# Kernel optimization log

Measured on AMD Instinct MI355X. Metric: run time of the kernel, lower is better.

## Reference

```python
import jax, jax.numpy as jnp
import numpy as np

P = 16        # patch size
IMG = 224     # image H=W
C = 3         # channels
D = 768       # projection_dim (= patch flatten dim here)
H = 12        # num heads
M = D // 4    # new_size = flattened_size / shrink_ratio(4) = 192
L = 6         # transformer layers
N = (IMG // P) ** 2   # 196 patches
FF = 3072     # dense_units[0]
HEAD = 512    # dense_units[2]
NCLS = 1000
EPS = 1e-6
B = 32


def setup_inputs() -> dict:
    key = jax.random.key(0)
    ks = iter(jax.random.split(key, 40))
    u = lambda shape, s=0.02: jax.random.uniform(next(ks), shape, jnp.float32, -s, s)
    image = jax.random.normal(next(ks), (B, IMG, IMG, C), jnp.float32)
    return dict(
        image=image,
        patch_w=u((P * P * C, D)), patch_b=u((D,)), pos_emb=u((N, D)),
        qw=u((L, D, M, H)), qb=jnp.zeros((L, M, H), jnp.float32),
        kw=u((L, D, M, H)), kb=jnp.zeros((L, M, H), jnp.float32),
        vw=u((L, D, M, H)), vb=jnp.zeros((L, M, H), jnp.float32),
        ow1=u((L, H * N, N)), ob1=jnp.zeros((L, M, N), jnp.float32),
        ow2=u((L, M, D)), ob2=jnp.zeros((L, N, D), jnp.float32),
        d1w=u((L, D, FF)), d1b=u((L, FF)),
        d2w=u((L, FF, D)), d2b=u((L, D)),
        head_w=u((N * D, HEAD), 0.005), head_b=u((HEAD,)),
        cls_w=u((HEAD, NCLS)), cls_b=u((NCLS,)),
    )


def _ln(x):
    # ViT_Custom_LayerNormalization: moments over axes [0,1,2] (all elements of [B,N,D])
    m = jnp.mean(x)
    v = jnp.mean(jnp.square(x - m))
    return (x - m) / jnp.sqrt(v + EPS)


def _gelu(x):
    return jax.nn.gelu(x, approximate=False)  # keras 'gelu' default is exact


def _forward(image, patch_w, patch_b, pos_emb, qw, qb, kw, kb, vw, vb,
             ow1, ob1, ow2, ob2, d1w, d1b, d2w, d2b, head_w, head_b, cls_w, cls_b):
    b = image.shape[0]
    # tf.image.extract_patches with VALID, stride=patch: [B,N,p*p*C] row-major patches
    patches = image.reshape(b, IMG // P, P, IMG // P, P, C)
    patches = patches.transpose(0, 1, 3, 2, 4, 5).reshape(b, N, P * P * C)
    x = patches @ patch_w + patch_b + pos_emb  # patch encode + pos embedding
    scale = 1.0 / np.float32(np.sqrt(D))       # key_dim = projection_dim
    for l in range(L):
        x1 = _ln(x)
        # per-head 3-D tensordot projections: [B,N,D] x [D,M,H] -> [B,N,M,H]
        q = jnp.einsum('bnd,dmh->bnmh', x1, qw[l]) + qb[l]
        k = jnp.einsum('bnd,dmh->bnmh', x1, kw[l]) + kb[l]
        v = jnp.einsum('bnd,dmh->bnmh', x1, vw[l]) + vb[l]
        att = jnp.einsum('bnmh,bNmh->bhnN', q, k) * scale  # [B,H,N,N]
        a = jax.nn.softmax(att, axis=-1)
        # attn @ V, then the module's transpose/unstack-concat -> [B,M,H*N] head-major
        o = jnp.einsum('bhnN,bNmh->bmhn', a, v).reshape(b, M, H * N)
        t = (o @ ow1[l] + ob1[l]).transpose(0, 2, 1)  # [B,N,M]
        attn_out = t @ ow2[l] + ob2[l]                # [B,N,D]
        x2 = attn_out + x
        x3 = _ln(x2)
        h = _gelu(x3 @ d1w[l] + d1b[l])
        h = _gelu(h @ d2w[l] + d2b[l])
        x = h + x2
    x = _ln(x)
    flat = x.reshape(b, N * D)
    feat = _gelu(flat @ head_w + head_b)
    return feat @ cls_w + cls_b  # [B, NCLS]


def reference(image, patch_w, patch_b, pos_emb, qw, qb, kw, kb, vw, vb,
              ow1, ob1, ow2, ob2, d1w, d1b, d2w, d2b, head_w, head_b, cls_w, cls_b):
    return _forward(image, patch_w, patch_b, pos_emb, qw, qb, kw, kb, vw, vb,
                    ow1, ob1, ow2, ob2, d1w, d1b, d2w, d2b, head_w, head_b, cls_w, cls_b)
```

## Files before the change

kernel.cpp:

```cpp
#include <hip/hip_runtime.h>
#include <cmath>

#define BZ    32
#define NP    196
#define DDIM  768
#define NHEAD 12
#define MDIM  192
#define NLAY  6
#define FFDIM 3072
#define HEADU 512
#define NCLS  1000
#define KHEAD 150528
#define BND   4816896

typedef __bf16 bf16_t;
typedef __bf16 bf16x8 __attribute__((ext_vector_type(8)));
typedef __bf16 bf16x4 __attribute__((ext_vector_type(4)));
typedef float  f32x4  __attribute__((ext_vector_type(4)));
typedef float  f32x2  __attribute__((ext_vector_type(2)));

#define OB_X      0L
#define OB_R      19267584L
#define OB_XB     38535168L
#define OB_XQKV   48168960L
#define OB_VT     134873088L
#define OB_O      165543936L
#define OB_T      194641920L
#define OB_WQKV   197050368L
#define OB_WO1    260751360L
#define OB_WO2    268025856L
#define OB_WD1    269795328L
#define OB_WD2    298106880L
#define OB_WPAT   326418432L
#define OB_BQKV   327598080L
#define OB_OB1T   327763968L
#define OB_RED    328667136L
#define OB_FEAT   328675584L

#define VT_SSTRIDE  39936L
#define ATTN_LDSP   93184
#define ATTN_LDS    143360
#define XROW        13824

__device__ __forceinline__ float gelu_exact(float x){
    return 0.5f * x * (1.0f + erff(x * 0.70710678118654752f));
}

__device__ __forceinline__ void gld16(const void* g, void* l){
    __builtin_amdgcn_global_load_lds((const __attribute__((address_space(1))) void*)g,
                                     (__attribute__((address_space(3))) void*)l, 16, 0, 0);
}

__global__ void __launch_bounds__(256)
patch_extract_k(const float* __restrict__ img, bf16_t* __restrict__ out)
{
    long idx = (long)blockIdx.x * 256 + threadIdx.x;
    if (idx >= (long)BND) return;
    int k = (int)(idx % DDIM);
    long bn = idx / DDIM;
    int n = (int)(bn % NP);
    int b = (int)(bn / NP);
    int c  = k % 3;
    int pj = (k / 3) % 16;
    int pi = k / 48;
    int gi = n / 14, gj = n % 14;
    long src = (((long)(b * 224 + gi * 16 + pi)) * 224 + (gj * 16 + pj)) * 3 + c;
    out[idx] = (bf16_t)img[src];
}

__global__ void __launch_bounds__(256)
wconv_k(const float* __restrict__ in, bf16_t* __restrict__ out,
        int IR, int IC, long OLD, int perm, int padTo, long inZ, long outZ)
{
    __shared__ float tile[32][33];
    int tid = threadIdx.x, tx = tid & 31, ty = tid >> 5;
    int c0 = blockIdx.x * 32, r0 = blockIdx.y * 32;
    const float* inz = in + (long)blockIdx.z * inZ;
    bf16_t* outz = out + (long)blockIdx.z * outZ;
    #pragma unroll
    for (int i = 0; i < 4; i++){
        int r = r0 + ty + 8*i, c = c0 + tx;
        tile[ty + 8*i][tx] = (r < IR && c < IC) ? inz[(long)r * IC + c] : 0.f;
    }
    __syncthreads();
    #pragma unroll
    for (int i = 0; i < 4; i++){
        int c = c0 + ty + 8*i, r = r0 + tx;
        if (c < IC && r < padTo){
            long pc = perm ? (long)(c % 12) * 192 + c / 12 : (long)c;
            outz[pc * OLD + r] = (bf16_t)tile[tx][ty + 8*i];
        }
    }
}

__global__ void __launch_bounds__(256)
gather_bias_k(const float* __restrict__ qb, const float* __restrict__ kb,
              const float* __restrict__ vb, float* __restrict__ out)
{
    int tid = blockIdx.x * 256 + threadIdx.x;
    int l = blockIdx.y;
    if (tid >= 6912) return;
    int g = tid / 2304, w = tid % 2304;
    int h = w / 192, m = w % 192;
    const float* src = (g == 0) ? qb : (g == 1) ? kb : vb;
    out[l*6912 + tid] = src[l*2304 + m * 12 + h];
}

__global__ void __launch_bounds__(256)
tr_bias_k(const float* __restrict__ ob1, float* __restrict__ out)
{
    int idx = blockIdx.x * 256 + threadIdx.x;
    int l = blockIdx.y;
    if (idx >= 37632) return;
    int n = idx / 192, m = idx - n*192;
    out[(long)l*37632 + idx] = ob1[(long)l*37632 + m*196 + n];
}

__global__ void __launch_bounds__(256)
zero_pad_o_k(bf16_t* __restrict__ o)
{
    int idx = blockIdx.x * 256 + threadIdx.x;
    if (idx >= 6144*16) return;
    int r = idx >> 4, j = idx & 15;
    o[(long)r * 2368 + 2352 + j] = (bf16_t)0.f;
}

__global__ void __launch_bounds__(256)
tr_v_k(const bf16_t* __restrict__ X, bf16_t* __restrict__ VT)
{
    __shared__ bf16_t tile[32][33];
    int tid = threadIdx.x, tx = tid & 31, ty = tid >> 5;
    int s = blockIdx.z, b = s & 31, h = s >> 5;
    int m0 = blockIdx.x * 32, n0 = blockIdx.y * 32;
    #pragma unroll
    for (int i = 0; i < 4; i++){
        int r = n0 + ty + 8*i, c = m0 + tx;
        tile[ty + 8*i][tx] = (r < 196) ?
            X[(long)(b*196 + r) * 6912 + 4608 + h*192 + c] : (bf16_t)0.f;
    }
    __syncthreads();
    #pragma unroll
    for (int i = 0; i < 4; i++){
        int m = m0 + ty + 8*i, n = n0 + tx;
        if (n < 208)
            VT[(long)s * VT_SSTRIDE + (long)m * 208 + n] = tile[tx][ty + 8*i];
    }
}

__global__ void __launch_bounds__(256)
reduce_k(const float* __restrict__ x, float* __restrict__ psum, float* __restrict__ psq)
{
    __shared__ float ss[256], sq[256];
    float s = 0.f, q = 0.f;
    const long n4 = BND / 4;
    const float4* x4 = (const float4*)x;
    for (long i = (long)blockIdx.x * 256 + threadIdx.x; i < n4; i += (long)gridDim.x * 256){
        float4 v = x4[i];
        s += v.x + v.y + v.z + v.w;
        q += v.x*v.x + v.y*v.y + v.z*v.z + v.w*v.w;
    }
    ss[threadIdx.x] = s; sq[threadIdx.x] = q;
    __syncthreads();
    for (int st = 128; st > 0; st >>= 1){
        if (threadIdx.x < st){ ss[threadIdx.x] += ss[threadIdx.x+st]; sq[threadIdx.x] += sq[threadIdx.x+st]; }
        __syncthreads();
    }
    if (threadIdx.x == 0){ psum[blockIdx.x] = ss[0]; psq[blockIdx.x] = sq[0]; }
}

__global__ void __launch_bounds__(256)
ln_apply_k(const float* __restrict__ x, bf16_t* __restrict__ yb, float* __restrict__ yf,
           const float* __restrict__ psum, const float* __restrict__ psq)
{
    __shared__ float sred[8];
    int tid = threadIdx.x;
    float s = 0.f, q = 0.f;
    for (int i = tid; i < 1024; i += 256){ s += psum[i]; q += psq[i]; }
    #pragma unroll
    for (int off = 32; off > 0; off >>= 1){ s += __shfl_xor(s, off); q += __shfl_xor(q, off); }
    if ((tid & 63) == 0){ sred[(tid>>6)*2] = s; sred[(tid>>6)*2+1] = q; }
    __syncthreads();
    s = sred[0] + sred[2] + sred[4] + sred[6];
    q = sred[1] + sred[3] + sred[5] + sred[7];
    float mean = s / (float)BND;
    float inv  = rsqrtf(q / (float)BND - mean*mean + 1e-6f);

    long i = (long)blockIdx.x * 256 + tid;
    if (i >= BND / 4) return;
    float4 v = ((const float4*)x)[i];
    v.x = (v.x - mean) * inv;
    v.y = (v.y - mean) * inv;
    v.z = (v.z - mean) * inv;
    v.w = (v.w - mean) * inv;
    bf16x4 o4 = { (bf16_t)v.x, (bf16_t)v.y, (bf16_t)v.z, (bf16_t)v.w };
    ((bf16x4*)yb)[i] = o4;
    if (yf) ((float4*)yf)[i] = v;
}

__global__ void __launch_bounds__(256)
attn_fused_k(const bf16_t* __restrict__ XQKV, const bf16_t* __restrict__ VT,
             bf16_t* __restrict__ O)
{
    extern __shared__ char lds[];
    const int tid = threadIdx.x, lane = tid & 63, w = tid >> 6;
    const int fr = lane & 15, kc = lane >> 4;
    const int s = blockIdx.y, qhalf = blockIdx.x;
    const int q0 = qhalf * 112;
    const int b = s & 31, h = s >> 5;
    const float scale = 0.03608439182435161f;
    const char* Xb = (const char*)XQKV + (long)(b*196) * XROW;
    const char* Qs = Xb + h*384;
    const char* Ks = Xb + 4608 + h*384;
    const char* Vs = (const char*)(VT + (long)s * VT_SSTRIDE);

    for (int t = 0; t < 23; t++){
        int idx = t*256 + tid;
        if (idx < 5824){
            int row = idx / 28, sl = idx - row*28;
            bool val = (sl < 24) && (row < 196);
            const char* src = Ks + (val ? ((long)row*XROW + ((sl*16) ^ ((row & 7) << 4))) : 0);
            gld16(src, lds + idx*16);
        }
    }
    asm volatile("s_waitcnt vmcnt(0)");
    __syncthreads();

    float pv_all[2][13][4];
    #pragma unroll
    for (int ii = 0; ii < 2; ii++){
        int i = w + ii*4;
        if (i >= 7) continue;
        f32x4 sa[13];
        #pragma unroll
        for (int f = 0; f < 13; f++) sa[f] = (f32x4){0.f,0.f,0.f,0.f};
        int qr = q0 + i*16 + fr; if (qr > 195) qr = 195;
        #pragma unroll
        for (int c = 0; c < 6; c++){
            bf16x8 av = *(const bf16x8*)(Qs + (long)qr*XROW + c*64 + kc*16);
            #pragma unroll
            for (int f = 0; f < 13; f++){
                int krow = f*16 + fr;
                bf16x8 bv = *(const bf16x8*)(lds + krow*448 + ((c*64 + kc*16) ^ ((krow & 7) << 4)));
                sa[f] = __builtin_amdgcn_mfma_f32_16x16x32_bf16(av, bv, sa[f], 0, 0, 0);
            }
        }
        #pragma unroll
        for (int r = 0; r < 4; r++){
            float mx = -1e30f;
            #pragma unroll
            for (int f = 0; f < 13; f++)
                if (f*16 + fr < 196) mx = fmaxf(mx, sa[f][r] * scale);
            mx = fmaxf(mx, __shfl_xor(mx, 1));
            mx = fmaxf(mx, __shfl_xor(mx, 2));
            mx = fmaxf(mx, __shfl_xor(mx, 4));
            mx = fmaxf(mx, __shfl_xor(mx, 8));
            float sum = 0.f;
            #pragma unroll
            for (int f = 0; f < 13; f++){
                float pv = (f*16 + fr < 196) ? __expf(sa[f][r] * scale - mx) : 0.f;
                pv_all[ii][f][r] = pv; sum += pv;
            }
            sum += __shfl_xor(sum, 1);
            sum += __shfl_xor(sum, 2);
            sum += __shfl_xor(sum, 4);
            sum += __shfl_xor(sum, 8);
            float inv = 1.f / sum;
            #pragma unroll
            for (int f = 0; f < 13; f++) pv_all[ii][f][r] *= inv;
        }
        #pragma unroll
        for (int f = 0; f < 13; f++)
            #pragma unroll
            for (int r = 0; r < 4; r++){
                int row = i*16 + kc*4 + r;
                int cb = (f*16 + fr) * 2;
                int a = ATTN_LDSP + row*448 + (cb < 384 ? (cb ^ ((row & 7) << 4)) : cb);
                *(bf16_t*)(lds + a) = (bf16_t)pv_all[ii][f][r];
            }
        if (lane < 32){
            int row = i*16 + (lane >> 1);
            *(f32x4*)(lds + ATTN_LDSP + row*448 + 416 + (lane & 1)*16) = (f32x4){0.f,0.f,0.f,0.f};
        }
    }
    __syncthreads();

    for (int t = 0; t < 21; t++){
        int idx = t*256 + tid;
        int row = idx / 28, sl = idx - row*28;
        bool val = (sl < 26);
        int cb = (sl < 24) ? ((sl*16) ^ ((row & 7) << 4)) : sl*16;
        const char* src = Vs + (val ? (row*416 + cb) : 0);
        gld16(src, lds + idx*16);
    }
    asm volatile("s_waitcnt vmcnt(0)");
    __syncthreads();

    f32x4 oa2[2][12];
    #pragma unroll
    for (int ii = 0; ii < 2; ii++){
        int i = w + ii*4;
        #pragma unroll
        for (int f = 0; f < 12; f++) oa2[ii][f] = (f32x4){0.f,0.f,0.f,0.f};
        if (i >= 7) continue;
        #pragma unroll
        for (int c = 0; c < 7; c++){
            int prow = i*16 + fr;
            int cb = c*64 + kc*16;
            int acb = (cb < 384) ? (cb ^ ((prow & 7) << 4)) : cb;
            bf16x8 av = *(const bf16x8*)(lds + ATTN_LDSP + prow*448 + acb);
            #pragma unroll
            for (int f = 0; f < 12; f++){
                int vrow = f*16 + fr;
                int bcb = (cb < 384) ? (cb ^ ((vrow & 7) << 4)) : cb;
                bf16x8 bv = *(const bf16x8*)(lds + vrow*448 + bcb);
                oa2[ii][f] = __builtin_amdgcn_mfma_f32_16x16x32_bf16(av, bv, oa2[ii][f], 0, 0, 0);
            }
        }
    }
    __syncthreads();

    #pragma unroll
    for (int ii = 0; ii < 2; ii++){
        int i = w + ii*4;
        if (i >= 7) continue;
        #pragma unroll
        for (int f = 0; f < 12; f++){
            int m = f*16 + fr;
            #pragma unroll
            for (int r = 0; r < 4; r++){
                int nl = i*16 + kc*4 + r;
                *(bf16_t*)(lds + m*232 + nl*2) = (bf16_t)oa2[ii][f][r];
            }
        }
    }
    __syncthreads();
    const int nch = (qhalf == 0) ? 28 : 21;
    const int total = 192 * nch;
    char* ob = (char*)O + ((long)(b*192))*4736 + ((long)(h*196 + q0))*2;
    for (int idx = tid; idx < total; idx += 256){
        int m = idx / nch, ch = idx - m*nch;
        f32x2 v2 = *(const f32x2*)(lds + m*232 + ch*8);
        *(f32x2*)(ob + (long)m*4736 + ch*8) = v2;
    }
}

__global__ void __launch_bounds__(256)
mfma_gemm_k(const bf16_t* __restrict__ A, long ldA, long sA,
            const bf16_t* __restrict__ B, long ldB, long sB,
            void* __restrict__ C, long ldC, long sC,
            const float* __restrict__ Cadd,
            const float* __restrict__ bias1,
            const float* __restrict__ bias2, int b2mod, int b2ld,
            int Md, int Nd, int Kd, float alpha, int doGelu, int mode)
{
    __shared__ bf16_t sm[3][2][128][32];
    const int tid = threadIdx.x;
    const int lane = tid & 63, w = tid >> 6;
    const int wm = w >> 1, wn = w & 1;
    const int z = blockIdx.z;

    int n2d = gridDim.x * gridDim.y;
    int flat = blockIdx.x + gridDim.x * blockIdx.y;
    int q8 = n2d >> 3, r8 = n2d & 7;
    int xcd = flat & 7, pos = flat >> 3;
    int id2 = (xcd < r8 ? xcd*(q8+1) : r8*(q8+1) + (xcd-r8)*q8) + pos;
    int bx = id2 % gridDim.x, by = id2 / gridDim.x;

    const int row0 = by * 128, col0 = bx * 128;

    const bf16_t* Ab = A + (long)z * sA + (long)row0 * ldA;
    const bf16_t* Bb = B + (long)z * sB + (long)col0 * ldB;

    f32x4 acc[4][4];
    #pragma unroll
    for (int i = 0; i < 4; i++)
        #pragma unroll
        for (int j = 0; j < 4; j++)
            acc[i][j] = (f32x4){0.f, 0.f, 0.f, 0.f};

    const int fr = lane & 15, kc = lane >> 4;
    const int swz = (fr >> 1) & 3;
    int aOff[4], bOff[4];
    #pragma unroll
    for (int i = 0; i < 4; i++){
        aOff[i] = (wm*64 + i*16 + fr) * 64 + ((kc ^ swz) << 4);
        bOff[i] = (wn*64 + i*16 + fr) * 64 + ((kc ^ swz) << 4);
    }

    auto stage = [&](int buf, int kt){
        long kOff = (long)kt * 32;
        #pragma unroll
        for (int r = 0; r < 2; r++){
            int idx = r*256 + tid;
            int row = idx >> 2, cp = idx & 3;
            int cc = cp ^ ((row >> 1) & 3);
            gld16((const void*)(Ab + (long)row*ldA + kOff + cc*8), (void*)&sm[buf][0][row][cp*8]);
            gld16((const void*)(Bb + (long)row*ldB + kOff + cc*8), (void*)&sm[buf][1][row][cp*8]);
        }
    };

    const int nt = Kd >> 5;
    stage(0, 0);
    stage(1, 1);
    asm volatile("s_waitcnt vmcnt(4)" ::: "memory");
    __builtin_amdgcn_s_barrier();
    __builtin_amdgcn_sched_barrier(0);

    for (int t = 0; t < nt; t++){
        int cur = t % 3;
        if (t + 2 < nt) stage((t + 2) % 3, t + 2);
        const char* baseA = (const char*)sm + cur * 16384;
        const char* baseB = baseA + 8192;
        bf16x8 av[4], bv[4];
        #pragma unroll
        for (int i = 0; i < 4; i++){
            av[i] = *(const bf16x8*)(baseA + aOff[i]);
            bv[i] = *(const bf16x8*)(baseB + bOff[i]);
        }
        __builtin_amdgcn_s_setprio(1);
        #pragma unroll
        for (int i = 0; i < 4; i++)
            #pragma unroll
            for (int j = 0; j < 4; j++)
                acc[i][j] = __builtin_amdgcn_mfma_f32_16x16x32_bf16(av[i], bv[j], acc[i][j], 0, 0, 0);
        __builtin_amdgcn_s_setprio(0);
        if (t + 2 < nt)      asm volatile("s_waitcnt vmcnt(4)" ::: "memory");
        else if (t + 1 < nt) asm volatile("s_waitcnt vmcnt(0)" ::: "memory");
        __builtin_amdgcn_s_barrier();
        __builtin_amdgcn_sched_barrier(0);
    }

    #pragma unroll
    for (int i = 0; i < 4; i++){
        int gmb = row0 + wm*64 + i*16 + kc*4;
        #pragma unroll
        for (int j = 0; j < 4; j++){
            int gn = col0 + wn*64 + j*16 + fr;
            if (gn >= Nd) continue;
            #pragma unroll
            for (int r = 0; r < 4; r++){
                int gm = gmb + r;
                if (gm >= Md) continue;
                float v = alpha * acc[i][j][r];
                if (bias1) v += bias1[gn];
                if (bias2) v += bias2[(long)(gm % b2mod) * b2ld + gn];
                if (doGelu) v = gelu_exact(v);
                if (mode == 0){
                    long off = (long)z*sC + (long)gm*ldC + gn;
                    if (Cadd) v += Cadd[off];
                    ((float*)C)[off] = v;
                } else {
                    ((bf16_t*)C)[(long)z*sC + (long)gm*ldC + gn] = (bf16_t)v;
                }
            }
        }
    }
}

__global__ void __launch_bounds__(256)
head_splitk_k(const float* __restrict__ A, const float* __restrict__ W, float* __restrict__ feat)
{
    __shared__ float As[16][36];
    __shared__ float Bs[16][68];
    int col0 = blockIdx.x * 64;
    long kbase = (long)blockIdx.y * 2352;
    int tid = threadIdx.x, tx = tid & 15, ty = tid >> 4;
    float acc[2][4] = {};
    for (int k0 = 0; k0 < 2352; k0 += 16){
        #pragma unroll
        for (int u = 0; u < 2; u++){
            int idx = tid * 2 + u;
            int m = idx >> 4, kk = idx & 15;
            As[kk][m] = A[(long)m * KHEAD + kbase + k0 + kk];
        }
        #pragma unroll
        for (int u = 0; u < 4; u++){
            int idx = tid * 4 + u;
            int kk = idx >> 6, n = idx & 63;
            Bs[kk][n] = W[(kbase + k0 + kk) * 512 + col0 + n];
        }
        __syncthreads();
        #pragma unroll
        for (int kk = 0; kk < 16; kk++){
            float a0 = As[kk][ty*2], a1 = As[kk][ty*2+1];
            float b0 = Bs[kk][tx*4], b1 = Bs[kk][tx*4+1], b2 = Bs[kk][tx*4+2], b3 = Bs[kk][tx*4+3];
            acc[0][0] += a0*b0; acc[0][1] += a0*b1; acc[0][2] += a0*b2; acc[0][3] += a0*b3;
            acc[1][0] += a1*b0; acc[1][1] += a1*b1; acc[1][2] += a1*b2; acc[1][3] += a1*b3;
        }
        __syncthreads();
    }
    #pragma unroll
    for (int i = 0; i < 2; i++)
        #pragma unroll
        for (int j = 0; j < 4; j++)
            atomicAdd(&feat[(ty*2 + i) * 512 + col0 + tx*4 + j], acc[i][j]);
}

__global__ void __launch_bounds__(256)
head_finish_k(float* __restrict__ feat, const float* __restrict__ hb)
{
    int i = blockIdx.x * 256 + threadIdx.x;
    if (i < BZ * HEADU) feat[i] = gelu_exact(feat[i] + hb[i & 511]);
}

__global__ void __launch_bounds__(256)
cls_k(const float* __restrict__ feat, const float* __restrict__ W,
      const float* __restrict__ bias, float* __restrict__ out)
{
    __shared__ float fs[512];
    int b = blockIdx.y;
    int j = blockIdx.x * 256 + threadIdx.x;
    for (int i = threadIdx.x; i < 512; i += 256) fs[i] = feat[b * 512 + i];
    __syncthreads();
    if (j < NCLS){
        float s = bias[j];
        for (int k = 0; k < 512; k++) s += fs[k] * W[(long)k * NCLS + j];
        out[b * NCLS + j] = s;
    }
}

extern "C" void kernel_launch(void* const* d_in, const int* in_sizes, int n_in,
                              void* d_out, int out_size, void* d_ws, size_t ws_size,
                              hipStream_t stream)
{
    const float* image   = (const float*)d_in[0];
    const float* patch_w = (const float*)d_in[1];
    const float* patch_b = (const float*)d_in[2];
    const float* pos_emb = (const float*)d_in[3];
    const float* qw  = (const float*)d_in[4];
    const float* qb  = (const float*)d_in[5];
    const float* kw  = (const float*)d_in[6];
    const float* kb  = (const float*)d_in[7];
    const float* vw  = (const float*)d_in[8];
    const float* vb  = (const float*)d_in[9];
    const float* ow1 = (const float*)d_in[10];
    const float* ob1 = (const float*)d_in[11];
    const float* ow2 = (const float*)d_in[12];
    const float* ob2 = (const float*)d_in[13];
    const float* d1w = (const float*)d_in[14];
    const float* d1b = (const float*)d_in[15];
    const float* d2w = (const float*)d_in[16];
    const float* d2b = (const float*)d_in[17];
    const float* head_w = (const float*)d_in[18];
    const float* head_b = (const float*)d_in[19];
    const float* cls_w  = (const float*)d_in[20];
    const float* cls_b  = (const float*)d_in[21];

    char* wsb = (char*)d_ws;
    float*  X    = (float*) (wsb + OB_X);
    float*  R    = (float*) (wsb + OB_R);
    bf16_t* XB   = (bf16_t*)(wsb + OB_XB);
    bf16_t* XQKV = (bf16_t*)(wsb + OB_XQKV);
    bf16_t* VT   = (bf16_t*)(wsb + OB_VT);
    bf16_t* O    = (bf16_t*)(wsb + OB_O);
    bf16_t* Tt   = (bf16_t*)(wsb + OB_T);
    bf16_t* H1   = XQKV;
    bf16_t* PATB = XQKV;
    bf16_t* WQKV = (bf16_t*)(wsb + OB_WQKV);
    bf16_t* WO1  = (bf16_t*)(wsb + OB_WO1);
    bf16_t* WO2  = (bf16_t*)(wsb + OB_WO2);
    bf16_t* WD1  = (bf16_t*)(wsb + OB_WD1);
    bf16_t* WD2  = (bf16_t*)(wsb + OB_WD2);
    bf16_t* WPAT = (bf16_t*)(wsb + OB_WPAT);
    float*  BQKV = (float*) (wsb + OB_BQKV);
    float*  OB1T = (float*) (wsb + OB_OB1T);
    float*  RSUM = (float*) (wsb + OB_RED);
    float*  RSQ  = RSUM + 1024;
    float*  FEAT = (float*) (wsb + OB_FEAT);
    float*  out  = (float*)d_out;

    hipFuncSetAttribute((const void*)attn_fused_k,
                        hipFuncAttributeMaxDynamicSharedMemorySize, ATTN_LDS);

    auto mg = [&](const bf16_t* A, long ldA, long sA, const bf16_t* B, long ldB, long sB,
                  void* C, long ldC, long sC, const float* Cadd, const float* b1,
                  const float* b2, int b2mod, int b2ld,
                  int Md, int Nd, int Kd, int nb, float alpha, int gelu, int mode){
        dim3 g((Nd + 127) / 128, (Md + 127) / 128, nb);
        mfma_gemm_k<<<g, 256, 0, stream>>>(A, ldA, sA, B, ldB, sB, C, ldC, sC,
                                           Cadd, b1, b2, b2mod, b2ld,
                                           Md, Nd, Kd, alpha, gelu, mode);
    };
    auto wconv = [&](const float* in, bf16_t* o_, int IR, int IC, int perm, long OLD,
                     int padTo, int nz, long inZ, long outZ){
        dim3 g((IC + 31) / 32, (padTo + 31) / 32, nz);
        wconv_k<<<g, 256, 0, stream>>>(in, o_, IR, IC, OLD, perm, padTo, inZ, outZ);
    };
    auto layernorm = [&](const float* in, bf16_t* ob, float* of){
        reduce_k<<<1024, 256, 0, stream>>>(in, RSUM, RSQ);
        ln_apply_k<<<4704, 256, 0, stream>>>(in, ob, of, RSUM, RSQ);
    };

    wconv(patch_w, WPAT, 768, 768, 0, 768, 768, 1, 0, 0);
    wconv(qw, WQKV,               768, 2304, 1, 768, 768, 6, 768L*2304, 6912L*768);
    wconv(kw, WQKV + 2304L*768,   768, 2304, 1, 768, 768, 6, 768L*2304, 6912L*768);
    wconv(vw, WQKV + 4608L*768,   768, 2304, 1, 768, 768, 6, 768L*2304, 6912L*768);
    wconv(ow1, WO1, 2352, 196, 0, 2368, 2368, 6, 2352L*196, 606208L);
    wconv(ow2, WO2, 192, 768, 0, 192, 192, 6, 147456L, 147456L);
    wconv(d1w, WD1, 768, 3072, 0, 768, 768, 6, 2359296L, 2359296L);
    wconv(d2w, WD2, 3072, 768, 0, 3072, 3072, 6, 2359296L, 2359296L);
    gather_bias_k<<<dim3(27, 6), 256, 0, stream>>>(qb, kb, vb, BQKV);
    tr_bias_k<<<dim3(147, 6), 256, 0, stream>>>(ob1, OB1T);

    patch_extract_k<<<18816, 256, 0, stream>>>(image, PATB);
    mg(PATB, 768, 0, WPAT, 768, 0, X, 768, 0,
       nullptr, patch_b, pos_emb, 196, 768, 6272, 768, 768, 1, 1.f, 0, 0);
    zero_pad_o_k<<<384, 256, 0, stream>>>(O);

    for (int l = 0; l < NLAY; l++){
        layernorm(X, XB, nullptr);
        mg(XB, 768, 0, WQKV + (long)l*6912*768, 768, 0, XQKV, 6912, 0, nullptr,
           BQKV + l*6912, nullptr, 1, 1, 6272, 6912, 768, 1, 1.f, 0, 1);
        tr_v_k<<<dim3(6, 7, 384), 256, 0, stream>>>(XQKV, VT);
        attn_fused_k<<<dim3(2, 384), 256, ATTN_LDS, stream>>>(XQKV, VT, O);
        mg(WO1 + (long)l*606208, 2368, 0, O, 2368, 192L*2368, Tt, 192, 37632,
           nullptr, nullptr, OB1T + (long)l*37632, 196, 192,
           196, 192, 2368, 32, 1.f, 0, 1);
        mg(Tt, 192, 0, WO2 + (long)l*147456, 192, 0, R, 768, 0, X, nullptr,
           ob2 + (long)l*196*768, 196, 768, 6272, 768, 192, 1, 1.f, 0, 0);
        layernorm(R, XB, nullptr);
        mg(XB, 768, 0, WD1 + (long)l*2359296, 768, 0, H1, 3072, 0, nullptr,
           d1b + l*3072, nullptr, 1, 1, 6272, 3072, 768, 1, 1.f, 1, 1);
        mg(H1, 3072, 0, WD2 + (long)l*2359296, 3072, 0, X, 768, 0, R,
           d2b + l*768, nullptr, 1, 1, 6272, 768, 3072, 1, 1.f, 1, 0);
    }

    layernorm(X, XB, R);
    hipMemsetAsync(FEAT, 0, BZ * HEADU * sizeof(float), stream);
    head_splitk_k<<<dim3(8, 64), 256, 0, stream>>>(R, head_w, FEAT);
    head_finish_k<<<64, 256, 0, stream>>>(FEAT, head_b);
    cls_k<<<dim3(4, 32), 256, 0, stream>>>(FEAT, cls_w, cls_b, out);
    (void)in_sizes; (void)n_in; (void)out_size; (void)ws_size;
}
```

Measured before the change: 3.426 ms.

## Fuse layernorm statistics into GEMM epilogues and add small-tile GEMM for ow1

Each fp32-output GEMM that produces the residual stream now accumulates per-block sum and sum-of-squares in its epilogue and writes partials, so the separate full-tensor reduction kernel before each layernorm is removed. The batched ow1 projection uses a new 64x64-tile MFMA kernel, which raises block count for the small 196x192 per-batch problem. The head GELU+bias is folded into the classifier kernel. The cost is extra epilogue work and a block-level sync in the main GEMM. The sum-of-squares variance is kept, and partials are now summed over 294 blocks.

```diff
diff --git a/kernel.cpp b/kernel.cpp
--- a/kernel.cpp
+++ b/kernel.cpp
@@ -12,6 +12,7 @@
 #define NCLS  1000
 #define KHEAD 150528
 #define BND   4816896
+#define NPART 294
 
 typedef __bf16 bf16_t;
 typedef __bf16 bf16x8 __attribute__((ext_vector_type(8)));
@@ -148,34 +149,13 @@
 }
 
 __global__ void __launch_bounds__(256)
-reduce_k(const float* __restrict__ x, float* __restrict__ psum, float* __restrict__ psq)
-{
-    __shared__ float ss[256], sq[256];
-    float s = 0.f, q = 0.f;
-    const long n4 = BND / 4;
-    const float4* x4 = (const float4*)x;
-    for (long i = (long)blockIdx.x * 256 + threadIdx.x; i < n4; i += (long)gridDim.x * 256){
-        float4 v = x4[i];
-        s += v.x + v.y + v.z + v.w;
-        q += v.x*v.x + v.y*v.y + v.z*v.z + v.w*v.w;
-    }
-    ss[threadIdx.x] = s; sq[threadIdx.x] = q;
-    __syncthreads();
-    for (int st = 128; st > 0; st >>= 1){
-        if (threadIdx.x < st){ ss[threadIdx.x] += ss[threadIdx.x+st]; sq[threadIdx.x] += sq[threadIdx.x+st]; }
-        __syncthreads();
-    }
-    if (threadIdx.x == 0){ psum[blockIdx.x] = ss[0]; psq[blockIdx.x] = sq[0]; }
-}
-
-__global__ void __launch_bounds__(256)
 ln_apply_k(const float* __restrict__ x, bf16_t* __restrict__ yb, float* __restrict__ yf,
-           const float* __restrict__ psum, const float* __restrict__ psq)
+           const float* __restrict__ psum, const float* __restrict__ psq, int npart)
 {
     __shared__ float sred[8];
     int tid = threadIdx.x;
     float s = 0.f, q = 0.f;
-    for (int i = tid; i < 1024; i += 256){ s += psum[i]; q += psq[i]; }
+    for (int i = tid; i < npart; i += 256){ s += psum[i]; q += psq[i]; }
     #pragma unroll
     for (int off = 32; off > 0; off >>= 1){ s += __shfl_xor(s, off); q += __shfl_xor(q, off); }
     if ((tid & 63) == 0){ sred[(tid>>6)*2] = s; sred[(tid>>6)*2+1] = q; }
@@ -351,9 +331,11 @@
             const float* __restrict__ Cadd,
             const float* __restrict__ bias1,
             const float* __restrict__ bias2, int b2mod, int b2ld,
-            int Md, int Nd, int Kd, float alpha, int doGelu, int mode)
+            int Md, int Nd, int Kd, float alpha, int doGelu, int mode,
+            float* __restrict__ psum, float* __restrict__ psq, int redN)
 {
     __shared__ bf16_t sm[3][2][128][32];
+    __shared__ float redbuf[8];
     const int tid = threadIdx.x;
     const int lane = tid & 63, w = tid >> 6;
     const int wm = w >> 1, wn = w & 1;
@@ -430,6 +412,7 @@
         __builtin_amdgcn_sched_barrier(0);
     }
 
+    float rs = 0.f, rq = 0.f;
     #pragma unroll
     for (int i = 0; i < 4; i++){
         int gmb = row0 + wm*64 + i*16 + kc*4;
@@ -449,9 +432,114 @@
                     long off = (long)z*sC + (long)gm*ldC + gn;
                     if (Cadd) v += Cadd[off];
                     ((float*)C)[off] = v;
+                    rs += v; rq += v*v;
                 } else {
                     ((bf16_t*)C)[(long)z*sC + (long)gm*ldC + gn] = (bf16_t)v;
                 }
+            }
+        }
+    }
+
+    if (redN > 0){
+        #pragma unroll
+        for (int off = 32; off > 0; off >>= 1){
+            rs += __shfl_xor(rs, off); rq += __shfl_xor(rq, off);
+        }
+        if (lane == 0){ redbuf[w] = rs; redbuf[4 + w] = rq; }
+        __syncthreads();
+        if (tid == 0){
+            psum[flat] = redbuf[0] + redbuf[1] + redbuf[2] + redbuf[3];
+            psq[flat]  = redbuf[4] + redbuf[5] + redbuf[6] + redbuf[7];
+        }
+    }
+}
+
+__global__ void __launch_bounds__(256)
+gemm64_k(const bf16_t* __restrict__ A, long ldA, long sA,
+         const bf16_t* __restrict__ B, long ldB, long sB,
+         bf16_t* __restrict__ C, long ldC, long sC,
+         const float* __restrict__ bias2, int b2ld,
+         int Md, int Nd, int Kd)
+{
+    __shared__ bf16_t sm[3][2][64][32];
+    const int tid = threadIdx.x;
+    const int lane = tid & 63, w = tid >> 6;
+    const int wm = w >> 1, wn = w & 1;
+    const int z = blockIdx.z;
+    const int row0 = blockIdx.y * 64, col0 = blockIdx.x * 64;
+
+    const bf16_t* Ab = A + (long)z * sA + (long)row0 * ldA;
+    const bf16_t* Bb = B + (long)z * sB + (long)col0 * ldB;
+
+    f32x4 acc[2][2];
+    #pragma unroll
+    for (int i = 0; i < 2; i++)
+        #pragma unroll
+        for (int j = 0; j < 2; j++)
+            acc[i][j] = (f32x4){0.f,0.f,0.f,0.f};
+
+    const int fr = lane & 15, kc = lane >> 4;
+    const int swz = (fr >> 1) & 3;
+    int aOff[2], bOff[2];
+    #pragma unroll
+    for (int i = 0; i < 2; i++){
+        aOff[i] = (wm*32 + i*16 + fr) * 64 + ((kc ^ swz) << 4);
+        bOff[i] = (wn*32 + i*16 + fr) * 64 + ((kc ^ swz) << 4);
+    }
+
+    auto stage = [&](int buf, int kt){
+        long kOff = (long)kt * 32;
+        int row = tid >> 2, cp = tid & 3;
+        int cc = cp ^ ((row >> 1) & 3);
+        gld16((const void*)(Ab + (long)row*ldA + kOff + cc*8), (void*)&sm[buf][0][row][cp*8]);
+        gld16((const void*)(Bb + (long)row*ldB + kOff + cc*8), (void*)&sm[buf][1][row][cp*8]);
+    };
+
+    const int nt = Kd >> 5;
+    stage(0, 0);
+    stage(1, 1);
+    asm volatile("s_waitcnt vmcnt(2)" ::: "memory");
+    __builtin_amdgcn_s_barrier();
+    __builtin_amdgcn_sched_barrier(0);
+
+    for (int t = 0; t < nt; t++){
+        int cur = t % 3;
+        if (t + 2 < nt) stage((t + 2) % 3, t + 2);
+        const char* baseA = (const char*)sm + cur * 8192;
+        const char* baseB = baseA + 4096;
+        bf16x8 av[2], bv[2];
+        #pragma unroll
+        for (int i = 0; i < 2; i++){
+            av[i] = *(const bf16x8*)(baseA + aOff[i]);
+            bv[i] = *(const bf16x8*)(baseB + bOff[i]);
+        }
+        __builtin_amdgcn_s_setprio(1);
+        #pragma unroll
+        for (int i = 0; i < 2; i++)
+            #pragma unroll
+            for (int j = 0; j < 2; j++)
+                acc[i][j] = __builtin_amdgcn_mfma_f32_16x16x32_bf16(av[i], bv[j], acc[i][j], 0, 0, 0);
+        __builtin_amdgcn_s_setprio(0);
+        if (t + 2 < nt)      asm volatile("s_waitcnt vmcnt(2)" ::: "memory");
+        else if (t + 1 < nt) asm volatile("s_waitcnt vmcnt(0)" ::: "memory");
+        __builtin_amdgcn_s_barrier();
+        __builtin_amdgcn_sched_barrier(0);
+    }
+
+    #pragma unroll
+    for (int i = 0; i < 2; i++){
+        int gmb = row0 + wm*32 + i*16 + kc*4;
+        #pragma unroll
+        for (int j = 0; j < 2; j++){
+            int gn = col0 + wn*32 + j*16 + fr;
+            if (gn >= Nd) continue;
+            #pragma unroll
+            for (int r = 0; r < 4; r++){
+                int gm = gmb + r;
+                if (gm >= Md) continue;
+                float v = acc[i][j][r];
+                if (bias2) v += bias2[(long)gm * b2ld + gn];
+                C[(long)z*sC + (long)gm*ldC + gn] = (bf16_t)v;
             }
         }
     }
@@ -497,20 +585,14 @@
 }
 
 __global__ void __launch_bounds__(256)
-head_finish_k(float* __restrict__ feat, const float* __restrict__ hb)
-{
-    int i = blockIdx.x * 256 + threadIdx.x;
-    if (i < BZ * HEADU) feat[i] = gelu_exact(feat[i] + hb[i & 511]);
-}
-
-__global__ void __launch_bounds__(256)
-cls_k(const float* __restrict__ feat, const float* __restrict__ W,
-      const float* __restrict__ bias, float* __restrict__ out)
+cls_k(const float* __restrict__ feat, const float* __restrict__ hb,
+      const float* __restrict__ W, const float* __restrict__ bias, float* __restrict__ out)
 {
     __shared__ float fs[512];
     int b = blockIdx.y;
     int j = blockIdx.x * 256 + threadIdx.x;
-    for (int i = threadIdx.x; i < 512; i += 256) fs[i] = feat[b * 512 + i];
+    for (int i = threadIdx.x; i < 512; i += 256)
+        fs[i] = gelu_exact(feat[b * 512 + i] + hb[i]);
     __syncthreads();
     if (j < NCLS){
         float s = bias[j];
@@ -564,8 +646,8 @@
     bf16_t* WPAT = (bf16_t*)(wsb + OB_WPAT);
     float*  BQKV = (float*) (wsb + OB_BQKV);
     float*  OB1T = (float*) (wsb + OB_OB1T);
-    float*  RSUM = (float*) (wsb + OB_RED);
-    float*  RSQ  = RSUM + 1024;
+    float*  PS   = (float*) (wsb + OB_RED);
+    float*  PQ   = PS + 512;
     float*  FEAT = (float*) (wsb + OB_FEAT);
     float*  out  = (float*)d_out;
 
@@ -575,20 +657,19 @@
     auto mg = [&](const bf16_t* A, long ldA, long sA, const bf16_t* B, long ldB, long sB,
                   void* C, long ldC, long sC, const float* Cadd, const float* b1,
                   const float* b2, int b2mod, int b2ld,
-                  int Md, int Nd, int Kd, int nb, float alpha, int gelu, int mode){
+                  int Md, int Nd, int Kd, int nb, float alpha, int gelu, int mode, int redN){
         dim3 g((Nd + 127) / 128, (Md + 127) / 128, nb);
         mfma_gemm_k<<<g, 256, 0, stream>>>(A, ldA, sA, B, ldB, sB, C, ldC, sC,
                                            Cadd, b1, b2, b2mod, b2ld,
-                                           Md, Nd, Kd, alpha, gelu, mode);
+                                           Md, Nd, Kd, alpha, gelu, mode, PS, PQ, redN);
     };
     auto wconv = [&](const float* in, bf16_t* o_, int IR, int IC, int perm, long OLD,
                      int padTo, int nz, long inZ, long outZ){
         dim3 g((IC + 31) / 32, (padTo + 31) / 32, nz);
         wconv_k<<<g, 256, 0, stream>>>(in, o_, IR, IC, OLD, perm, padTo, inZ, outZ);
     };
-    auto layernorm = [&](const float* in, bf16_t* ob, float* of){
-        reduce_k<<<1024, 256, 0, stream>>>(in, RSUM, RSQ);
-        ln_apply_k<<<4704, 256, 0, stream>>>(in, ob, of, RSUM, RSQ);
+    auto lnapply = [&](const float* in, bf16_t* ob, float* of){
+        ln_apply_k<<<4704, 256, 0, stream>>>(in, ob, of, PS, PQ, NPART);
     };
 
     wconv(patch_w, WPAT, 768, 768, 0, 768, 768, 1, 0, 0);
@@ -604,31 +685,30 @@
 
     patch_extract_k<<<18816, 256, 0, stream>>>(image, PATB);
     mg(PATB, 768, 0, WPAT, 768, 0, X, 768, 0,
-       nullptr, patch_b, pos_emb, 196, 768, 6272, 768, 768, 1, 1.f, 0, 0);
+       nullptr, patch_b, pos_emb, 196, 768, 6272, 768, 768, 1, 1.f, 0, 0, NPART);
     zero_pad_o_k<<<384, 256, 0, stream>>>(O);
 
     for (int l = 0; l < NLAY; l++){
-        layernorm(X, XB, nullptr);
+        lnapply(X, XB, nullptr);
         mg(XB, 768, 0, WQKV + (long)l*6912*768, 768, 0, XQKV, 6912, 0, nullptr,
-           BQKV + l*6912, nullptr, 1, 1, 6272, 6912, 768, 1, 1.f, 0, 1);
+           BQKV + l*6912, nullptr, 1, 1, 6272, 6912, 768, 1, 1.f, 0, 1, 0);
         tr_v_k<<<dim3(6, 7, 384), 256, 0, stream>>>(XQKV, VT);
         attn_fused_k<<<dim3(2, 384), 256, ATTN_LDS, stream>>>(XQKV, VT, O);
-        mg(WO1 + (long)l*606208, 2368, 0, O, 2368, 192L*2368, Tt, 192, 37632,
-           nullptr, nullptr, OB1T + (long)l*37632, 196, 192,
-           196, 192, 2368, 32, 1.f, 0, 1);
+        gemm64_k<<<dim3(3, 4, 32), 256, 0, stream>>>(
+            WO1 + (long)l*606208, 2368, 0, O, 2368, 192L*2368, Tt, 192, 37632,
+            OB1T + (long)l*37632, 192, 196, 192, 2368);
         mg(Tt, 192, 0, WO2 + (long)l*147456, 192, 0, R, 768, 0, X, nullptr,
-           ob2 + (long)l*196*768, 196, 768, 6272, 768, 192, 1, 1.f, 0, 0);
-        layernorm(R, XB, nullptr);
+           ob2 + (long)l*196*768, 196, 768, 6272, 768, 192, 1, 1.f, 0, 0, NPART);
+        lnapply(R, XB, nullptr);
         mg(XB, 768, 0, WD1 + (long)l*2359296, 768, 0, H1, 3072, 0, nullptr,
-           d1b + l*3072, nullptr, 1, 1, 6272, 3072, 768, 1, 1.f, 1, 1);
+           d1b + l*3072, nullptr, 1, 1, 6272, 3072, 768, 1, 1.f, 1, 1, 0);
         mg(H1, 3072, 0, WD2 + (long)l*2359296, 3072, 0, X, 768, 0, R,
-           d2b + l*768, nullptr, 1, 1, 6272, 768, 3072, 1, 1.f, 1, 0);
-    }
-
-    layernorm(X, XB, R);
+           d2b + l*768, nullptr, 1, 1, 6272, 768, 3072, 1, 1.f, 1, 0, NPART);
+    }
+
+    lnapply(X, XB, R);
     hipMemsetAsync(FEAT, 0, BZ * HEADU * sizeof(float), stream);
     head_splitk_k<<<dim3(8, 64), 256, 0, stream>>>(R, head_w, FEAT);
-    head_finish_k<<<64, 256, 0, stream>>>(FEAT, head_b);
-    cls_k<<<dim3(4, 32), 256, 0, stream>>>(FEAT, cls_w, cls_b, out);
+    cls_k<<<dim3(4, 32), 256, 0, stream>>>(FEAT, head_b, cls_w, cls_b, out);
     (void)in_sizes; (void)n_in; (void)out_size; (void)ws_size;
 }
```

Result: no change. 3.459 ms (+1.0%).
